# Performance work log

Hardware: AMD Instinct MI355X
Metric: run time of the kernel (lower is better)

## Reference

```python
import jax, jax.numpy as jnp
import numpy as np

N = 40000    # nodes
E = 400000   # edges
H = 128      # hidden_channels
G = 50       # num_gaussians
L = 3        # num_interactions
NG = 256     # number of graphs in the batch
CUTOFF = 6.0


def setup_inputs() -> dict:
    key = jax.random.key(0)
    ks = jax.random.split(key, 16)

    def w(k, shape, fan_in):
        return (jax.random.normal(k, shape, jnp.float32) / np.float32(np.sqrt(fan_in)))

    inp = {}
    inp["atomic_numbers"] = jax.random.randint(ks[0], (N,), 0, 100)
    inp["pos"] = jax.random.normal(ks[1], (N, 3), jnp.float32) * 5.0
    inp["edge_index"] = jax.random.randint(ks[2], (2, E), 0, N)
    inp["batch_ids"] = jnp.sort(jax.random.randint(ks[3], (N,), 0, NG))
    inp["embed"] = w(ks[4], (100, H), 1.0)
    inp["msg_w1"] = w(ks[5], (L, H, H), H)
    inp["msg_b1"] = jnp.zeros((L, H), jnp.float32)
    inp["msg_w2"] = w(ks[6], (L, H, 3 * H), H)
    inp["msg_b2"] = jnp.zeros((L, 3 * H), jnp.float32)
    inp["filt_w"] = w(ks[7], (L, G, 3 * H), G)
    inp["filt_b"] = jnp.zeros((L, 3 * H), jnp.float32)
    inp["vec_w"] = w(ks[8], (L, H, 2 * H), H)
    inp["upd_w1"] = w(ks[9], (L, 2 * H, H), 2 * H)
    inp["upd_b1"] = jnp.zeros((L, H), jnp.float32)
    inp["upd_w2"] = w(ks[10], (L, H, 3 * H), H)
    inp["upd_b2"] = jnp.zeros((L, 3 * H), jnp.float32)
    inp["ro_w1"] = w(ks[11], (H, H // 2), H)
    inp["ro_b1"] = jnp.zeros((H // 2,), jnp.float32)
    inp["ro_w2"] = w(ks[12], (H // 2, 1), H // 2)
    inp["ro_b2"] = jnp.zeros((1,), jnp.float32)
    return inp


def _painn(atomic_numbers, pos, edge_index, batch_ids, embed,
           msg_w1, msg_b1, msg_w2, msg_b2, filt_w, filt_b, vec_w,
           upd_w1, upd_b1, upd_w2, upd_b2, ro_w1, ro_b1, ro_w2, ro_b2):
    src, dst = edge_index[0], edge_index[1]
    n = atomic_numbers.shape[0]

    # geometry
    dvec = pos[src] - pos[dst]                              # [E,3]
    dist = jnp.linalg.norm(dvec, axis=-1)                   # [E]
    dvec_n = dvec / (dist[:, None] + 1e-8)                  # [E,3]

    # Gaussian smearing (RBF expansion of distances)
    offset = jnp.linspace(0.0, CUTOFF, G).astype(jnp.float32)
    coeff = -0.5 / (offset[1] - offset[0]) ** 2
    rbf = jnp.exp(coeff * (dist[:, None] - offset[None, :]) ** 2)  # [E,G]

    s = embed[atomic_numbers]                               # [N,H]
    v = jnp.zeros((n, 3, H), s.dtype)                       # [N,3,H]

    for i in range(L):
        # --- message block ---
        w = rbf @ filt_w[i] + filt_b[i]                     # [E,3H]
        s_all = jax.nn.relu(s @ msg_w1[i] + msg_b1[i]) @ msg_w2[i] + msg_b2[i]  # [N,3H]
        gate = s_all[src] * w                               # [E,3H]
        g0, g1, g2 = jnp.split(gate, 3, axis=-1)            # each [E,H]
        ds_e = g0
        dv_e = v[src] * g1[:, None, :] + dvec_n[:, :, None] * g2[:, None, :]  # [E,3,H]
        ds = jax.ops.segment_sum(ds_e, dst, num_segments=n)
        dv = jax.ops.segment_sum(dv_e, dst, num_segments=n)
        s = s + ds
        v = v + dv

        # --- update block ---
        vt = v @ vec_w[i]                                   # [N,3,2H]
        V1, V2 = jnp.split(vt, 2, axis=-1)                  # [N,3,H] each
        v_norm = jnp.linalg.norm(V1, axis=1)                # [N,H]
        u = (jax.nn.relu(jnp.concatenate([s, v_norm], axis=-1) @ upd_w1[i] + upd_b1[i])
             @ upd_w2[i] + upd_b2[i])                       # [N,3H]
        a, b, c = jnp.split(u, 3, axis=-1)
        s = s + a
        v = v * b[:, None, :] + V2 * c[:, None, :]

    # readout + global mean pool
    y = jax.nn.relu(s @ ro_w1 + ro_b1) @ ro_w2 + ro_b2      # [N,1]
    summed = jax.ops.segment_sum(y, batch_ids, num_segments=NG)
    counts = jax.ops.segment_sum(jnp.ones((n, 1), y.dtype), batch_ids, num_segments=NG)
    return summed / jnp.maximum(counts, 1.0)                # [NG,1]


def reference(atomic_numbers, pos, edge_index, batch_ids, embed,
              msg_w1, msg_b1, msg_w2, msg_b2, filt_w, filt_b, vec_w,
              upd_w1, upd_b1, upd_w2, upd_b2, ro_w1, ro_b1, ro_w2, ro_b2):
    return _painn(atomic_numbers, pos, edge_index, batch_ids, embed,
                  msg_w1, msg_b1, msg_w2, msg_b2, filt_w, filt_b, vec_w,
                  upd_w1, upd_b1, upd_w2, upd_b2, ro_w1, ro_b1, ro_w2, ro_b2)
```

## Files before the change

kernel.cpp:

```cpp
#include <hip/hip_runtime.h>
#include <hip/hip_bf16.h>
#include <math.h>


#define N_NODES 40000
#define N_EDGES 400000
#define NGAUSS  50
#define NLAY    3
#define NGRAPH  256

#define WS_BYTES (448ull * 1024 * 1024)
__device__ __align__(256) unsigned char g_ws[WS_BYTES];

typedef __attribute__((ext_vector_type(8))) short short8;
typedef __attribute__((ext_vector_type(4))) float f32x4;

__device__ __forceinline__ float relu_f(float x) { return fmaxf(x, 0.f); }
__device__ __forceinline__ unsigned short f2b(float x) {
  __hip_bfloat16 h = __float2bfloat16(x);
  return *reinterpret_cast<unsigned short*>(&h);
}
__device__ __forceinline__ float b2f(unsigned short u) {
  return __uint_as_float(((unsigned int)u) << 16);
}
__device__ __forceinline__ float b2f_lo(unsigned int u) {
  return __uint_as_float(u << 16);
}
__device__ __forceinline__ float b2f_hi(unsigned int u) {
  return __uint_as_float(u & 0xffff0000u);
}
__device__ __forceinline__ unsigned int pk(float a, float b) {
  return (unsigned int)f2b(a) | ((unsigned int)f2b(b) << 16);
}
__device__ __forceinline__ int perm384(int c) {
  int j = c >> 7, cc = c & 127;
  return (cc >> 1) * 6 + j * 2 + (cc & 1);
}

#define S0 (NLAY * 128 * 128)
#define S1 (NLAY * 128 * 384)
#define S2 (NLAY * 128 * 256)
#define S3 (NLAY * 256 * 128)
#define S4 (NLAY * 128 * 384)
#define S5 (NLAY * NGAUSS * 384)
#define S6 (128 * 64)
#define S7 (NLAY * 384)
#define S_TOT (S0 + S1 + S2 + S3 + S4 + S5 + S6 + S7)

__global__ __launch_bounds__(256) void cvt_all_kernel(
    const float* __restrict__ m1i, const float* __restrict__ m2i,
    const float* __restrict__ vwi, const float* __restrict__ u1i,
    const float* __restrict__ u2i, const float* __restrict__ fwi,
    const float* __restrict__ roi, const float* __restrict__ mb2i,
    unsigned short* __restrict__ m1o, unsigned short* __restrict__ m2o,
    unsigned short* __restrict__ vwo, unsigned short* __restrict__ u1o,
    unsigned short* __restrict__ u2o, unsigned short* __restrict__ fwo,
    unsigned short* __restrict__ roo, float* __restrict__ mb2o) {
  int i = blockIdx.x * 256 + threadIdx.x;
  if (i >= S_TOT) return;
  if (i < S0) { m1o[i] = f2b(m1i[i]); return; }
  i -= S0;
  if (i < S1) {
    int l = i / (128 * 384), rem = i % (128 * 384);
    int r = rem / 384, c = rem % 384;
    m2o[(size_t)l * 128 * 384 + r * 384 + perm384(c)] = f2b(m2i[i]);
    return;
  }
  i -= S1;
  if (i < S2) { vwo[i] = f2b(vwi[i]); return; }
  i -= S2;
  if (i < S3) { u1o[i] = f2b(u1i[i]); return; }
  i -= S3;
  if (i < S4) { u2o[i] = f2b(u2i[i]); return; }
  i -= S4;
  if (i < S5) {
    int l = i / (NGAUSS * 384), rem = i % (NGAUSS * 384);
    int g = rem / 384, c = rem % 384;
    fwo[(size_t)l * NGAUSS * 384 + g * 384 + perm384(c)] = f2b(fwi[i]);
    return;
  }
  i -= S5;
  if (i < S6) { roo[i] = f2b(roi[i]); return; }
  i -= S6;
  {
    int l = i / 384, c = i % 384;
    mb2o[l * 384 + perm384(c)] = mb2i[i];
  }
}

__global__ __launch_bounds__(256) void geom_kernel(const int* __restrict__ src,
                                                   const int* __restrict__ dst,
                                                   const float* __restrict__ pos,
                                                   float4* __restrict__ geom) {
  int e = blockIdx.x * 256 + threadIdx.x;
  if (e >= N_EDGES) return;
  int s = src[e], d = dst[e];
  float dx = pos[s * 3 + 0] - pos[d * 3 + 0];
  float dy = pos[s * 3 + 1] - pos[d * 3 + 1];
  float dz = pos[s * 3 + 2] - pos[d * 3 + 2];
  float dist = sqrtf(dx * dx + dy * dy + dz * dz);
  float inv = 1.f / (dist + 1e-8f);
  geom[e] = make_float4(dx * inv, dy * inv, dz * inv, dist);
}

__global__ __launch_bounds__(256) void hist_kernel(const int* __restrict__ dst,
                                                   int* __restrict__ deg) {
  int e = blockIdx.x * 256 + threadIdx.x;
  if (e < N_EDGES) atomicAdd(&deg[dst[e]], 1);
}

#define SCAN_NB ((N_NODES + 255) / 256)
__global__ __launch_bounds__(256) void scan_a(const int* __restrict__ deg,
                                              int* __restrict__ bsum) {
  __shared__ int red[4];
  int b = blockIdx.x, t = threadIdx.x;
  int i = b * 256 + t;
  int x = (i < N_NODES) ? deg[i] : 0;
#pragma unroll
  for (int o = 32; o > 0; o >>= 1) x += __shfl_xor(x, o);
  if ((t & 63) == 0) red[t >> 6] = x;
  __syncthreads();
  if (t == 0) bsum[b] = red[0] + red[1] + red[2] + red[3];
}

__global__ __launch_bounds__(64) void scan_b(const int* __restrict__ bsum,
                                             int* __restrict__ boff) {
  int lane = threadIdx.x;
  int carry = 0;
  for (int base = 0; base < SCAN_NB; base += 64) {
    int i = base + lane;
    int v = (i < SCAN_NB) ? bsum[i] : 0;
    int x = v;
#pragma unroll
    for (int d = 1; d < 64; d <<= 1) {
      int y = __shfl_up(x, d);
      if (lane >= d) x += y;
    }
    if (i < SCAN_NB) boff[i] = carry + x - v;
    carry += __shfl(x, 63);
  }
}

__global__ __launch_bounds__(256) void scan_c(const int* __restrict__ deg,
                                              const int* __restrict__ boff,
                                              int* __restrict__ off) {
  __shared__ int woff[4];
  int b = blockIdx.x, t = threadIdx.x, lane = t & 63, w = t >> 6;
  int i = b * 256 + t;
  int v = (i < N_NODES) ? deg[i] : 0;
  int x = v;
#pragma unroll
  for (int d = 1; d < 64; d <<= 1) {
    int y = __shfl_up(x, d);
    if (lane >= d) x += y;
  }
  if (lane == 63) woff[w] = x;
  __syncthreads();
  int add = 0;
  for (int k = 0; k < w; ++k) add += woff[k];
  if (i < N_NODES) off[i] = boff[b] + add + x - v;
  if (b == 0 && t == 0) off[N_NODES] = N_EDGES;
}

__global__ __launch_bounds__(256) void fill_kernel(const int* __restrict__ src,
                                                   const int* __restrict__ dst,
                                                   const int* __restrict__ off,
                                                   int* __restrict__ cursor,
                                                   const float4* __restrict__ geom,
                                                   int* __restrict__ srcs,
                                                   float4* __restrict__ geoms) {
  int e = blockIdx.x * 256 + threadIdx.x;
  if (e >= N_EDGES) return;
  int d = dst[e];
  int p = atomicAdd(&cursor[d], 1);
  int pos = off[d] + p;
  srcs[pos] = src[e];
  geoms[pos] = geom[e];
}

__global__ __launch_bounds__(256) void init_kernel(const int* __restrict__ z,
                                                   const float* __restrict__ embed,
                                                   float* __restrict__ s,
                                                   unsigned short* __restrict__ sb,
                                                   unsigned short* __restrict__ vax) {
  int idx = blockIdx.x * 256 + threadIdx.x;
  if (idx < N_NODES * 384) vax[idx] = 0;
  if (idx < N_NODES * 128) {
    int node = idx >> 7, c = idx & 127;
    float val = embed[z[node] * 128 + c];
    s[idx] = val;
    sb[idx] = f2b(val);
  }
}

template <int BN, int KT>
__global__ __launch_bounds__(256) void gemm_bf16(
    const unsigned short* __restrict__ A1, int lda1,
    const unsigned short* __restrict__ A2, int lda2, int kSplit,
    const unsigned short* __restrict__ B, int ldb,
    const float* __restrict__ bias,
    void* __restrict__ C, int ldc, int M, int K, int doRelu, int outMode) {
  constexpr int NF = BN / 16;
  constexpr int CT = BN / 4;
  __shared__ unsigned int Bt32[BN][KT / 2 + 4];
  int t = threadIdx.x;
  int lane = t & 63, w = t >> 6;
  int n0 = blockIdx.x * BN, m0 = blockIdx.y * 128;
  {
    int c4 = (t & (CT - 1)) * 4;
    int kstep = 2 * (256 / CT);
    for (int k = (t / CT) * 2; k < K; k += kstep) {
      uint2 va = *(const uint2*)&B[(size_t)k * ldb + n0 + c4];
      uint2 vb = *(const uint2*)&B[(size_t)(k + 1) * ldb + n0 + c4];
      Bt32[c4 + 0][k >> 1] = (va.x & 0xffffu) | (vb.x << 16);
      Bt32[c4 + 1][k >> 1] = (va.x >> 16) | (vb.x & 0xffff0000u);
      Bt32[c4 + 2][k >> 1] = (va.y & 0xffffu) | (vb.y << 16);
      Bt32[c4 + 3][k >> 1] = (va.y >> 16) | (vb.y & 0xffff0000u);
    }
  }
  __syncthreads();

  int row = lane & 15;
  int kg = lane >> 4;

  f32x4 acc[2][NF];
#pragma unroll
  for (int rf = 0; rf < 2; ++rf)
#pragma unroll
    for (int nf = 0; nf < NF; ++nf) acc[rf][nf] = (f32x4){0.f, 0.f, 0.f, 0.f};

  for (int ks = 0; ks < K; ks += 32) {
    int kk = ks + kg * 8;
    short8 af[2];
#pragma unroll
    for (int rf = 0; rf < 2; ++rf) {
      int mrow = m0 + w * 32 + rf * 16 + row;
      if (mrow >= M) mrow = M - 1;
      const unsigned short* Ap;
      int kloc;
      if (kk < kSplit) { Ap = A1 + (size_t)mrow * lda1; kloc = kk; }
      else             { Ap = A2 + (size_t)mrow * lda2; kloc = kk - kSplit; }
      af[rf] = *(const short8*)&Ap[kloc];
    }
#pragma unroll
    for (int nf = 0; nf < NF; ++nf) {
      short8 bf = *(const short8*)((const unsigned short*)Bt32[nf * 16 + row] + kk);
#pragma unroll
      for (int rf = 0; rf < 2; ++rf)
        acc[rf][nf] = __builtin_amdgcn_mfma_f32_16x16x32_bf16(af[rf], bf,
                                                              acc[rf][nf], 0, 0, 0);
    }
  }

#pragma unroll
  for (int rf = 0; rf < 2; ++rf)
#pragma unroll
    for (int nf = 0; nf < NF; ++nf)
#pragma unroll
      for (int r = 0; r < 4; ++r) {
        int gr = m0 + w * 32 + rf * 16 + kg * 4 + r;
        int gc = n0 + nf * 16 + row;
        if (gr < M) {
          float val = acc[rf][nf][r] + (bias ? bias[gc] : 0.f);
          if (doRelu) val = relu_f(val);
          if (outMode == 0) ((float*)C)[(size_t)gr * ldc + gc] = val;
          else              ((unsigned short*)C)[(size_t)gr * ldc + gc] = f2b(val);
        }
      }
}

__global__ __launch_bounds__(256) void msg_kernel(const int* __restrict__ off,
                                                  const int* __restrict__ srcs,
                                                  const float4* __restrict__ geoms,
                                                  const unsigned int* __restrict__ s_allX,
                                                  const unsigned int* __restrict__ fwX,
                                                  const float* __restrict__ fb,
                                                  const float* __restrict__ s_in,
                                                  const unsigned int* __restrict__ vAx,
                                                  float* __restrict__ s_out,
                                                  unsigned short* __restrict__ s_out_b,
                                                  unsigned short* __restrict__ v_out_b) {
  int node = blockIdx.x * 4 + (threadIdx.x >> 6);
  if (node >= N_NODES) return;
  int lane = threadIdx.x & 63;
  int c2 = lane * 2;
  const float DELTA = 6.0f / 49.0f;
  const float INVD = 49.0f / 6.0f;
  const float CO = -0.5f * INVD * INVD;
  float fbr[3][2];
#pragma unroll
  for (int jj = 0; jj < 3; ++jj) {
    float2 f = *(const float2*)&fb[jj * 128 + c2];
    fbr[jj][0] = f.x; fbr[jj][1] = f.y;
  }
  float ds[2] = {0.f, 0.f};
  float dv[3][2] = {{0.f}};
  int e0 = off[node], e1 = off[node + 1];

  for (int q = e0; q < e1; ++q) {
    int s = srcs[q];
    float4 gm = geoms[q];
    float d = gm.w;
    float wv[3][2];
#pragma unroll
    for (int jj = 0; jj < 3; ++jj) { wv[jj][0] = fbr[jj][0]; wv[jj][1] = fbr[jj][1]; }
    int glo = max(0, (int)ceilf(d * INVD - 8.f));
    int ghi = min(NGAUSS - 1, (int)floorf(d * INVD + 8.f));
    for (int g = glo; g <= ghi; ++g) {
      float diff = d - g * DELTA;
      float r = __expf(CO * diff * diff);
      const unsigned int* fr = fwX + g * 192 + lane * 3;
      unsigned int f0 = fr[0], f1 = fr[1], f2v = fr[2];
      wv[0][0] = fmaf(r, b2f_lo(f0), wv[0][0]);
      wv[0][1] = fmaf(r, b2f_hi(f0), wv[0][1]);
      wv[1][0] = fmaf(r, b2f_lo(f1), wv[1][0]);
      wv[1][1] = fmaf(r, b2f_hi(f1), wv[1][1]);
      wv[2][0] = fmaf(r, b2f_lo(f2v), wv[2][0]);
      wv[2][1] = fmaf(r, b2f_hi(f2v), wv[2][1]);
    }
    const unsigned int* ps = s_allX + (size_t)s * 192 + lane * 3;
    const unsigned int* pv = vAx + (size_t)s * 192 + lane * 3;
    unsigned int s0 = ps[0], s1 = ps[1], s2 = ps[2];
    unsigned int v0 = pv[0], v1 = pv[1], v2 = pv[2];
    float gt[3][2];
    gt[0][0] = b2f_lo(s0) * wv[0][0];
    gt[0][1] = b2f_hi(s0) * wv[0][1];
    gt[1][0] = b2f_lo(s1) * wv[1][0];
    gt[1][1] = b2f_hi(s1) * wv[1][1];
    gt[2][0] = b2f_lo(s2) * wv[2][0];
    gt[2][1] = b2f_hi(s2) * wv[2][1];
    ds[0] += gt[0][0];
    ds[1] += gt[0][1];
    float dn[3] = {gm.x, gm.y, gm.z};
    unsigned int vvs[3] = {v0, v1, v2};
#pragma unroll
    for (int dd = 0; dd < 3; ++dd) {
      dv[dd][0] = fmaf(b2f_lo(vvs[dd]), gt[1][0], fmaf(dn[dd], gt[2][0], dv[dd][0]));
      dv[dd][1] = fmaf(b2f_hi(vvs[dd]), gt[1][1], fmaf(dn[dd], gt[2][1], dv[dd][1]));
    }
  }

  size_t sb = (size_t)node * 128 + c2;
  float2 si = *(const float2*)&s_in[sb];
  float2 so = make_float2(si.x + ds[0], si.y + ds[1]);
  *(float2*)&s_out[sb] = so;
  *(unsigned int*)&s_out_b[sb] = pk(so.x, so.y);
  const unsigned int* pv0 = vAx + (size_t)node * 192 + lane * 3;
  unsigned int vi0 = pv0[0], vi1 = pv0[1], vi2 = pv0[2];
  unsigned int vis[3] = {vi0, vi1, vi2};
#pragma unroll
  for (int dd = 0; dd < 3; ++dd) {
    size_t vb = (size_t)node * 384 + dd * 128 + c2;
    float vo0 = b2f_lo(vis[dd]) + dv[dd][0];
    float vo1 = b2f_hi(vis[dd]) + dv[dd][1];
    *(unsigned int*)&v_out_b[vb] = pk(vo0, vo1);
  }
}

__global__ __launch_bounds__(256) void vnorm_kernel(const unsigned short* __restrict__ V12b,
                                                    unsigned short* __restrict__ vnb) {
  int idx = blockIdx.x * 256 + threadIdx.x;
  if (idx >= N_NODES * 32) return;
  int node = idx >> 5, c4 = (idx & 31) * 4;
  size_t b = (size_t)node * 768 + c4;
  ushort4 x = *(const ushort4*)&V12b[b];
  ushort4 y = *(const ushort4*)&V12b[b + 256];
  ushort4 zz = *(const ushort4*)&V12b[b + 512];
  ushort4 o;
  o.x = f2b(sqrtf(b2f(x.x) * b2f(x.x) + b2f(y.x) * b2f(y.x) + b2f(zz.x) * b2f(zz.x)));
  o.y = f2b(sqrtf(b2f(x.y) * b2f(x.y) + b2f(y.y) * b2f(y.y) + b2f(zz.y) * b2f(zz.y)));
  o.z = f2b(sqrtf(b2f(x.z) * b2f(x.z) + b2f(y.z) * b2f(y.z) + b2f(zz.z) * b2f(zz.z)));
  o.w = f2b(sqrtf(b2f(x.w) * b2f(x.w) + b2f(y.w) * b2f(y.w) + b2f(zz.w) * b2f(zz.w)));
  *(ushort4*)&vnb[(size_t)node * 128 + c4] = o;
}

__global__ __launch_bounds__(256) void update_kernel(const float* __restrict__ s_msg,
                                                     const unsigned short* __restrict__ v_msg_b,
                                                     const unsigned short* __restrict__ u_b,
                                                     const unsigned short* __restrict__ V12b,
                                                     float* __restrict__ s_out,
                                                     unsigned short* __restrict__ s_out_b,
                                                     unsigned int* __restrict__ vAx) {
  int idx = blockIdx.x * 256 + threadIdx.x;
  if (idx >= N_NODES * 32) return;
  int node = idx >> 5, c4 = (idx & 31) * 4;
  size_t ub = (size_t)node * 384 + c4;
  ushort4 a4 = *(const ushort4*)&u_b[ub];
  ushort4 b4 = *(const ushort4*)&u_b[ub + 128];
  ushort4 c4v = *(const ushort4*)&u_b[ub + 256];
  size_t sb = (size_t)node * 128 + c4;
  float4 sm = *(const float4*)&s_msg[sb];
  float4 so = make_float4(sm.x + b2f(a4.x), sm.y + b2f(a4.y),
                          sm.z + b2f(a4.z), sm.w + b2f(a4.w));
  *(float4*)&s_out[sb] = so;
  ushort4 sob = {f2b(so.x), f2b(so.y), f2b(so.z), f2b(so.w)};
  *(ushort4*)&s_out_b[sb] = sob;
  float bb[4] = {b2f(b4.x), b2f(b4.y), b2f(b4.z), b2f(b4.w)};
  float cc[4] = {b2f(c4v.x), b2f(c4v.y), b2f(c4v.z), b2f(c4v.w)};
  int l0 = c4 >> 1;
#pragma unroll
  for (int dd = 0; dd < 3; ++dd) {
    size_t vb = (size_t)node * 384 + dd * 128 + c4;
    size_t vbv = (size_t)node * 768 + dd * 256 + 128 + c4;
    ushort4 vm = *(const ushort4*)&v_msg_b[vb];
    ushort4 v2 = *(const ushort4*)&V12b[vbv];
    float o0 = b2f(vm.x) * bb[0] + b2f(v2.x) * cc[0];
    float o1 = b2f(vm.y) * bb[1] + b2f(v2.y) * cc[1];
    float o2 = b2f(vm.z) * bb[2] + b2f(v2.z) * cc[2];
    float o3 = b2f(vm.w) * bb[3] + b2f(v2.w) * cc[3];
    vAx[(size_t)node * 192 + l0 * 3 + dd] = pk(o0, o1);
    vAx[(size_t)node * 192 + (l0 + 1) * 3 + dd] = pk(o2, o3);
  }
}

__global__ __launch_bounds__(256) void readout2_kernel(const float* __restrict__ ro_h,
                                                       const float* __restrict__ w2,
                                                       float* __restrict__ y) {
  int node = blockIdx.x * 4 + (threadIdx.x >> 6);
  if (node >= N_NODES) return;
  int lane = threadIdx.x & 63;
  float v = ro_h[(size_t)node * 64 + lane] * w2[lane];
#pragma unroll
  for (int o = 32; o > 0; o >>= 1) v += __shfl_xor(v, o);
  if (lane == 0) y[node] = v;
}

__global__ __launch_bounds__(64) void pool_kernel(const float* __restrict__ y,
                                                  const int* __restrict__ batch,
                                                  const float* __restrict__ b2,
                                                  float* __restrict__ out) {
  int g = blockIdx.x;
  int lane = threadIdx.x;
  int s, e;
  {
    int lo = 0, hi = N_NODES;
    while (lo < hi) { int mid = (lo + hi) >> 1; if (batch[mid] < g) lo = mid + 1; else hi = mid; }
    s = lo;
    lo = s; hi = N_NODES;
    while (lo < hi) { int mid = (lo + hi) >> 1; if (batch[mid] < g + 1) lo = mid + 1; else hi = mid; }
    e = lo;
  }
  float acc = 0.f;
  for (int i = s + lane; i < e; i += 64) acc += y[i];
#pragma unroll
  for (int o = 32; o > 0; o >>= 1) acc += __shfl_xor(acc, o);
  if (lane == 0) {
    float c = (float)(e - s);
    out[g] = (acc + c * b2[0]) / fmaxf(c, 1.f);
  }
}

extern "C" void kernel_launch(void* const* d_in, const int* in_sizes, int n_in,
                              void* d_out, int out_size, void* d_ws, size_t ws_size,
                              hipStream_t stream) {
  const int*   z      = (const int*)d_in[0];
  const float* pos    = (const float*)d_in[1];
  const int*   esrc   = (const int*)d_in[2];
  const int*   edst   = esrc + N_EDGES;
  const int*   batch  = (const int*)d_in[3];
  const float* embed  = (const float*)d_in[4];
  const float* msg_w1 = (const float*)d_in[5];
  const float* msg_b1 = (const float*)d_in[6];
  const float* msg_w2 = (const float*)d_in[7];
  const float* msg_b2 = (const float*)d_in[8];
  const float* filt_w = (const float*)d_in[9];
  const float* filt_b = (const float*)d_in[10];
  const float* vec_w  = (const float*)d_in[11];
  const float* upd_w1 = (const float*)d_in[12];
  const float* upd_b1 = (const float*)d_in[13];
  const float* upd_w2 = (const float*)d_in[14];
  const float* upd_b2 = (const float*)d_in[15];
  const float* ro_w1  = (const float*)d_in[16];
  const float* ro_b1  = (const float*)d_in[17];
  const float* ro_w2  = (const float*)d_in[18];
  const float* ro_b2  = (const float*)d_in[19];
  (void)in_sizes; (void)n_in; (void)out_size;

  void* wsp = nullptr;
  if (hipGetSymbolAddress(&wsp, HIP_SYMBOL(g_ws)) != hipSuccess || wsp == nullptr) {
    wsp = d_ws;
  }
  char* wsb = (char*)wsp;
  size_t o = 0;
  auto alloc = [&](size_t bytes) -> void* {
    void* p = wsb + o;
    o += (bytes + 255) & ~(size_t)255;
    return p;
  };
  float4* geom   = (float4*)alloc(sizeof(float4) * N_EDGES);
  float4* geoms  = (float4*)alloc(sizeof(float4) * N_EDGES);
  int* srcs      = (int*)alloc(4ull * N_EDGES);
  int* csr_off   = (int*)alloc(4ull * (N_NODES + 1));
  int* deg       = (int*)alloc(4ull * N_NODES);
  int* cursor    = (int*)alloc(4ull * N_NODES);
  int* bsum      = (int*)alloc(4ull * SCAN_NB);
  int* boff      = (int*)alloc(4ull * SCAN_NB);
  float* sA      = (float*)alloc(4ull * N_NODES * 128);
  float* sB      = (float*)alloc(4ull * N_NODES * 128);
  float* ro_h    = (float*)alloc(4ull * N_NODES * 64);
  float* ybuf    = (float*)alloc(4ull * N_NODES);
  float* mb2p    = (float*)alloc(4ull * NLAY * 384);
  unsigned short* s_allX = (unsigned short*)alloc(2ull * N_NODES * 384);
  unsigned short* sAb    = (unsigned short*)alloc(2ull * N_NODES * 128);
  unsigned short* sBb    = (unsigned short*)alloc(2ull * N_NODES * 128);
  unsigned short* vAx    = (unsigned short*)alloc(2ull * N_NODES * 384);
  unsigned short* vBb    = (unsigned short*)alloc(2ull * N_NODES * 384);
  unsigned short* vnb    = (unsigned short*)alloc(2ull * N_NODES * 128);
  unsigned short* hidden = (unsigned short*)alloc(2ull * N_NODES * 128);
  unsigned short* Vbuf_b = (unsigned short*)alloc(2ull * N_NODES * 768);
  unsigned short* ubuf_b = (unsigned short*)alloc(2ull * N_NODES * 384);
  unsigned short* wb_m1  = (unsigned short*)alloc(2ull * S0);
  unsigned short* wb_m2  = (unsigned short*)alloc(2ull * S1);
  unsigned short* wb_vw  = (unsigned short*)alloc(2ull * S2);
  unsigned short* wb_u1  = (unsigned short*)alloc(2ull * S3);
  unsigned short* wb_u2  = (unsigned short*)alloc(2ull * S4);
  unsigned short* wb_fwX = (unsigned short*)alloc(2ull * S5);
  unsigned short* wb_ro  = (unsigned short*)alloc(2ull * S6);

  if (wsb == (char*)d_ws && o > ws_size) return;

  hipMemsetAsync(deg, 0, 4ull * N_NODES, stream);
  hipMemsetAsync(cursor, 0, 4ull * N_NODES, stream);

  cvt_all_kernel<<<(S_TOT + 255) / 256, 256, 0, stream>>>(
      msg_w1, msg_w2, vec_w, upd_w1, upd_w2, filt_w, ro_w1, msg_b2,
      wb_m1, wb_m2, wb_vw, wb_u1, wb_u2, wb_fwX, wb_ro, mb2p);

  geom_kernel<<<(N_EDGES + 255) / 256, 256, 0, stream>>>(esrc, edst, pos, geom);
  hist_kernel<<<(N_EDGES + 255) / 256, 256, 0, stream>>>(edst, deg);
  scan_a<<<SCAN_NB, 256, 0, stream>>>(deg, bsum);
  scan_b<<<1, 64, 0, stream>>>(bsum, boff);
  scan_c<<<SCAN_NB, 256, 0, stream>>>(deg, boff, csr_off);
  fill_kernel<<<(N_EDGES + 255) / 256, 256, 0, stream>>>(esrc, edst, csr_off, cursor,
                                                         geom, srcs, geoms);
  init_kernel<<<(N_NODES * 384 + 255) / 256, 256, 0, stream>>>(z, embed, sA, sAb, vAx);

  const int BIG = 1 << 30;
  const int GY40 = (N_NODES + 127) / 128;
  const int GY120 = (N_NODES * 3 + 127) / 128;
  for (int i = 0; i < NLAY; ++i) {
    const float* mb1 = msg_b1 + (size_t)i * 128;
    const float* mb2i = mb2p + (size_t)i * 384;
    const float* fbv = filt_b + (size_t)i * 384;
    const float* ub1 = upd_b1 + (size_t)i * 128;
    const float* ub2 = upd_b2 + (size_t)i * 384;
    const unsigned short* m1 = wb_m1 + (size_t)i * 128 * 128;
    const unsigned short* m2 = wb_m2 + (size_t)i * 128 * 384;
    const unsigned short* vw = wb_vw + (size_t)i * 128 * 256;
    const unsigned short* u1 = wb_u1 + (size_t)i * 256 * 128;
    const unsigned short* u2 = wb_u2 + (size_t)i * 128 * 384;
    const unsigned int* fwX = (const unsigned int*)(wb_fwX + (size_t)i * 50 * 384);

    gemm_bf16<64, 128><<<dim3(2, GY40), 256, 0, stream>>>(sAb, 128, sAb, 128, BIG, m1,
                                                          128, mb1, hidden, 128,
                                                          N_NODES, 128, 1, 1);
    gemm_bf16<128, 128><<<dim3(3, GY40), 256, 0, stream>>>(hidden, 128, hidden, 128,
                                                           BIG, m2, 384, mb2i, s_allX,
                                                           384, N_NODES, 128, 0, 1);
    msg_kernel<<<N_NODES / 4, 256, 0, stream>>>(csr_off, srcs, geoms,
                                                (const unsigned int*)s_allX, fwX, fbv,
                                                sA, (const unsigned int*)vAx,
                                                sB, sBb, vBb);
    gemm_bf16<128, 128><<<dim3(2, GY120), 256, 0, stream>>>(vBb, 128, vBb, 128, BIG,
                                                            vw, 256, nullptr, Vbuf_b,
                                                            256, N_NODES * 3, 128,
                                                            0, 1);
    vnorm_kernel<<<(N_NODES * 32 + 255) / 256, 256, 0, stream>>>(Vbuf_b, vnb);
    gemm_bf16<64, 256><<<dim3(2, GY40), 256, 0, stream>>>(sBb, 128, vnb, 128, 128, u1,
                                                          128, ub1, hidden, 128,
                                                          N_NODES, 256, 1, 1);
    gemm_bf16<128, 128><<<dim3(3, GY40), 256, 0, stream>>>(hidden, 128, hidden, 128,
                                                           BIG, u2, 384, ub2, ubuf_b,
                                                           384, N_NODES, 128, 0, 1);
    update_kernel<<<(N_NODES * 32 + 255) / 256, 256, 0, stream>>>(sB, vBb, ubuf_b,
                                                                  Vbuf_b, sA, sAb,
                                                                  (unsigned int*)vAx);
  }

  gemm_bf16<64, 128><<<dim3(1, GY40), 256, 0, stream>>>(sAb, 128, sAb, 128, BIG, wb_ro,
                                                        64, ro_b1, ro_h, 64, N_NODES,
                                                        128, 1, 0);
  readout2_kernel<<<N_NODES / 4, 256, 0, stream>>>(ro_h, wb_ro ? ro_w2 : ro_w2, ybuf);
  pool_kernel<<<NGRAPH, 64, 0, stream>>>(ybuf, batch, ro_b2, (float*)d_out);
}
```

Before: 1.103 ms.

## Interleave scalar filter and vector features per node; fuse geometry into CSR fill

The per-node scalar message features and vector state now share one interleaved buffer (768 bf16 per node), so each gathered neighbour in the message kernel reads one contiguous 1.5KB region instead of two separate rows. The geometry kernel is folded into the CSR fill kernel, which removes one launch and an intermediate float4 edge array. The trade-off is a wider row stride for the GEMM output and for vector writes in the update kernel, and an unused parameter left in the message kernel.

Result: no change. 1.089 ms (-1.2%).

```diff
diff --git a/kernel.cpp b/kernel.cpp
--- a/kernel.cpp
+++ b/kernel.cpp
@@ -88,10 +88,72 @@
   }
 }
 
-__global__ __launch_bounds__(256) void geom_kernel(const int* __restrict__ src,
+__global__ __launch_bounds__(256) void hist_kernel(const int* __restrict__ dst,
+                                                   int* __restrict__ deg) {
+  int e = blockIdx.x * 256 + threadIdx.x;
+  if (e < N_EDGES) atomicAdd(&deg[dst[e]], 1);
+}
+
+#define SCAN_NB ((N_NODES + 255) / 256)
+__global__ __launch_bounds__(256) void scan_a(const int* __restrict__ deg,
+                                              int* __restrict__ bsum) {
+  __shared__ int red[4];
+  int b = blockIdx.x, t = threadIdx.x;
+  int i = b * 256 + t;
+  int x = (i < N_NODES) ? deg[i] : 0;
+#pragma unroll
+  for (int o = 32; o > 0; o >>= 1) x += __shfl_xor(x, o);
+  if ((t & 63) == 0) red[t >> 6] = x;
+  __syncthreads();
+  if (t == 0) bsum[b] = red[0] + red[1] + red[2] + red[3];
+}
+
+__global__ __launch_bounds__(64) void scan_b(const int* __restrict__ bsum,
+                                             int* __restrict__ boff) {
+  int lane = threadIdx.x;
+  int carry = 0;
+  for (int base = 0; base < SCAN_NB; base += 64) {
+    int i = base + lane;
+    int v = (i < SCAN_NB) ? bsum[i] : 0;
+    int x = v;
+#pragma unroll
+    for (int d = 1; d < 64; d <<= 1) {
+      int y = __shfl_up(x, d);
+      if (lane >= d) x += y;
+    }
+    if (i < SCAN_NB) boff[i] = carry + x - v;
+    carry += __shfl(x, 63);
+  }
+}
+
+__global__ __launch_bounds__(256) void scan_c(const int* __restrict__ deg,
+                                              const int* __restrict__ boff,
+                                              int* __restrict__ off) {
+  __shared__ int woff[4];
+  int b = blockIdx.x, t = threadIdx.x, lane = t & 63, w = t >> 6;
+  int i = b * 256 + t;
+  int v = (i < N_NODES) ? deg[i] : 0;
+  int x = v;
+#pragma unroll
+  for (int d = 1; d < 64; d <<= 1) {
+    int y = __shfl_up(x, d);
+    if (lane >= d) x += y;
+  }
+  if (lane == 63) woff[w] = x;
+  __syncthreads();
+  int add = 0;
+  for (int k = 0; k < w; ++k) add += woff[k];
+  if (i < N_NODES) off[i] = boff[b] + add + x - v;
+  if (b == 0 && t == 0) off[N_NODES] = N_EDGES;
+}
+
+__global__ __launch_bounds__(256) void fill_kernel(const int* __restrict__ src,
                                                    const int* __restrict__ dst,
+                                                   const int* __restrict__ off,
+                                                   int* __restrict__ cursor,
                                                    const float* __restrict__ pos,
-                                                   float4* __restrict__ geom) {
+                                                   int* __restrict__ srcs,
+                                                   float4* __restrict__ geoms) {
   int e = blockIdx.x * 256 + threadIdx.x;
   if (e >= N_EDGES) return;
   int s = src[e], d = dst[e];
@@ -100,91 +162,22 @@
   float dz = pos[s * 3 + 2] - pos[d * 3 + 2];
   float dist = sqrtf(dx * dx + dy * dy + dz * dz);
   float inv = 1.f / (dist + 1e-8f);
-  geom[e] = make_float4(dx * inv, dy * inv, dz * inv, dist);
-}
-
-__global__ __launch_bounds__(256) void hist_kernel(const int* __restrict__ dst,
-                                                   int* __restrict__ deg) {
-  int e = blockIdx.x * 256 + threadIdx.x;
-  if (e < N_EDGES) atomicAdd(&deg[dst[e]], 1);
-}
-
-#define SCAN_NB ((N_NODES + 255) / 256)
-__global__ __launch_bounds__(256) void scan_a(const int* __restrict__ deg,
-                                              int* __restrict__ bsum) {
-  __shared__ int red[4];
-  int b = blockIdx.x, t = threadIdx.x;
-  int i = b * 256 + t;
-  int x = (i < N_NODES) ? deg[i] : 0;
-#pragma unroll
-  for (int o = 32; o > 0; o >>= 1) x += __shfl_xor(x, o);
-  if ((t & 63) == 0) red[t >> 6] = x;
-  __syncthreads();
-  if (t == 0) bsum[b] = red[0] + red[1] + red[2] + red[3];
-}
-
-__global__ __launch_bounds__(64) void scan_b(const int* __restrict__ bsum,
-                                             int* __restrict__ boff) {
-  int lane = threadIdx.x;
-  int carry = 0;
-  for (int base = 0; base < SCAN_NB; base += 64) {
-    int i = base + lane;
-    int v = (i < SCAN_NB) ? bsum[i] : 0;
-    int x = v;
-#pragma unroll
-    for (int d = 1; d < 64; d <<= 1) {
-      int y = __shfl_up(x, d);
-      if (lane >= d) x += y;
-    }
-    if (i < SCAN_NB) boff[i] = carry + x - v;
-    carry += __shfl(x, 63);
-  }
-}
-
-__global__ __launch_bounds__(256) void scan_c(const int* __restrict__ deg,
-                                              const int* __restrict__ boff,
-                                              int* __restrict__ off) {
-  __shared__ int woff[4];
-  int b = blockIdx.x, t = threadIdx.x, lane = t & 63, w = t >> 6;
-  int i = b * 256 + t;
-  int v = (i < N_NODES) ? deg[i] : 0;
-  int x = v;
-#pragma unroll
-  for (int d = 1; d < 64; d <<= 1) {
-    int y = __shfl_up(x, d);
-    if (lane >= d) x += y;
-  }
-  if (lane == 63) woff[w] = x;
-  __syncthreads();
-  int add = 0;
-  for (int k = 0; k < w; ++k) add += woff[k];
-  if (i < N_NODES) off[i] = boff[b] + add + x - v;
-  if (b == 0 && t == 0) off[N_NODES] = N_EDGES;
-}
-
-__global__ __launch_bounds__(256) void fill_kernel(const int* __restrict__ src,
-                                                   const int* __restrict__ dst,
-                                                   const int* __restrict__ off,
-                                                   int* __restrict__ cursor,
-                                                   const float4* __restrict__ geom,
-                                                   int* __restrict__ srcs,
-                                                   float4* __restrict__ geoms) {
-  int e = blockIdx.x * 256 + threadIdx.x;
-  if (e >= N_EDGES) return;
-  int d = dst[e];
   int p = atomicAdd(&cursor[d], 1);
-  int pos = off[d] + p;
-  srcs[pos] = src[e];
-  geoms[pos] = geom[e];
+  int q = off[d] + p;
+  srcs[q] = s;
+  geoms[q] = make_float4(dx * inv, dy * inv, dz * inv, dist);
 }
 
 __global__ __launch_bounds__(256) void init_kernel(const int* __restrict__ z,
                                                    const float* __restrict__ embed,
                                                    float* __restrict__ s,
                                                    unsigned short* __restrict__ sb,
-                                                   unsigned short* __restrict__ vax) {
+                                                   unsigned short* __restrict__ sv) {
   int idx = blockIdx.x * 256 + threadIdx.x;
-  if (idx < N_NODES * 384) vax[idx] = 0;
+  if (idx < N_NODES * 384) {
+    int node = idx / 384, c = idx % 384;
+    sv[(size_t)node * 768 + 384 + c] = 0;
+  }
   if (idx < N_NODES * 128) {
     int node = idx >> 7, c = idx & 127;
     float val = embed[z[node] * 128 + c];
@@ -272,14 +265,14 @@
 __global__ __launch_bounds__(256) void msg_kernel(const int* __restrict__ off,
                                                   const int* __restrict__ srcs,
                                                   const float4* __restrict__ geoms,
-                                                  const unsigned int* __restrict__ s_allX,
+                                                  const unsigned int* __restrict__ sv,
                                                   const unsigned int* __restrict__ fwX,
                                                   const float* __restrict__ fb,
                                                   const float* __restrict__ s_in,
-                                                  const unsigned int* __restrict__ vAx,
                                                   float* __restrict__ s_out,
                                                   unsigned short* __restrict__ s_out_b,
-                                                  unsigned short* __restrict__ v_out_b) {
+                                                  unsigned short* __restrict__ v_out_b,
+                                                  unsigned int* __restrict__ sv_v_out) {
   int node = blockIdx.x * 4 + (threadIdx.x >> 6);
   if (node >= N_NODES) return;
   int lane = threadIdx.x & 63;
@@ -318,10 +311,9 @@
       wv[2][0] = fmaf(r, b2f_lo(f2v), wv[2][0]);
       wv[2][1] = fmaf(r, b2f_hi(f2v), wv[2][1]);
     }
-    const unsigned int* ps = s_allX + (size_t)s * 192 + lane * 3;
-    const unsigned int* pv = vAx + (size_t)s * 192 + lane * 3;
-    unsigned int s0 = ps[0], s1 = ps[1], s2 = ps[2];
-    unsigned int v0 = pv[0], v1 = pv[1], v2 = pv[2];
+    const unsigned int* base = sv + (size_t)s * 384 + lane * 3;
+    unsigned int s0 = base[0], s1 = base[1], s2 = base[2];
+    unsigned int v0 = base[192], v1 = base[193], v2 = base[194];
     float gt[3][2];
     gt[0][0] = b2f_lo(s0) * wv[0][0];
     gt[0][1] = b2f_hi(s0) * wv[0][1];
@@ -345,7 +337,7 @@
   float2 so = make_float2(si.x + ds[0], si.y + ds[1]);
   *(float2*)&s_out[sb] = so;
   *(unsigned int*)&s_out_b[sb] = pk(so.x, so.y);
-  const unsigned int* pv0 = vAx + (size_t)node * 192 + lane * 3;
+  const unsigned int* pv0 = sv + (size_t)node * 384 + 192 + lane * 3;
   unsigned int vi0 = pv0[0], vi1 = pv0[1], vi2 = pv0[2];
   unsigned int vis[3] = {vi0, vi1, vi2};
 #pragma unroll
@@ -355,6 +347,7 @@
     float vo1 = b2f_hi(vis[dd]) + dv[dd][1];
     *(unsigned int*)&v_out_b[vb] = pk(vo0, vo1);
   }
+  (void)sv_v_out;
 }
 
 __global__ __launch_bounds__(256) void vnorm_kernel(const unsigned short* __restrict__ V12b,
@@ -380,7 +373,7 @@
                                                      const unsigned short* __restrict__ V12b,
                                                      float* __restrict__ s_out,
                                                      unsigned short* __restrict__ s_out_b,
-                                                     unsigned int* __restrict__ vAx) {
+                                                     unsigned int* __restrict__ sv) {
   int idx = blockIdx.x * 256 + threadIdx.x;
   if (idx >= N_NODES * 32) return;
   int node = idx >> 5, c4 = (idx & 31) * 4;
@@ -408,8 +401,8 @@
     float o1 = b2f(vm.y) * bb[1] + b2f(v2.y) * cc[1];
     float o2 = b2f(vm.z) * bb[2] + b2f(v2.z) * cc[2];
     float o3 = b2f(vm.w) * bb[3] + b2f(v2.w) * cc[3];
-    vAx[(size_t)node * 192 + l0 * 3 + dd] = pk(o0, o1);
-    vAx[(size_t)node * 192 + (l0 + 1) * 3 + dd] = pk(o2, o3);
+    sv[(size_t)node * 384 + 192 + l0 * 3 + dd] = pk(o0, o1);
+    sv[(size_t)node * 384 + 192 + (l0 + 1) * 3 + dd] = pk(o2, o3);
   }
 }
 
@@ -487,7 +480,6 @@
     o += (bytes + 255) & ~(size_t)255;
     return p;
   };
-  float4* geom   = (float4*)alloc(sizeof(float4) * N_EDGES);
   float4* geoms  = (float4*)alloc(sizeof(float4) * N_EDGES);
   int* srcs      = (int*)alloc(4ull * N_EDGES);
   int* csr_off   = (int*)alloc(4ull * (N_NODES + 1));
@@ -500,10 +492,9 @@
   float* ro_h    = (float*)alloc(4ull * N_NODES * 64);
   float* ybuf    = (float*)alloc(4ull * N_NODES);
   float* mb2p    = (float*)alloc(4ull * NLAY * 384);
-  unsigned short* s_allX = (unsigned short*)alloc(2ull * N_NODES * 384);
+  unsigned short* svX    = (unsigned short*)alloc(2ull * N_NODES * 768);
   unsigned short* sAb    = (unsigned short*)alloc(2ull * N_NODES * 128);
   unsigned short* sBb    = (unsigned short*)alloc(2ull * N_NODES * 128);
-  unsigned short* vAx    = (unsigned short*)alloc(2ull * N_NODES * 384);
   unsigned short* vBb    = (unsigned short*)alloc(2ull * N_NODES * 384);
   unsigned short* vnb    = (unsigned short*)alloc(2ull * N_NODES * 128);
   unsigned short* hidden = (unsigned short*)alloc(2ull * N_NODES * 128);
@@ -526,14 +517,13 @@
       msg_w1, msg_w2, vec_w, upd_w1, upd_w2, filt_w, ro_w1, msg_b2,
       wb_m1, wb_m2, wb_vw, wb_u1, wb_u2, wb_fwX, wb_ro, mb2p);
 
-  geom_kernel<<<(N_EDGES + 255) / 256, 256, 0, stream>>>(esrc, edst, pos, geom);
   hist_kernel<<<(N_EDGES + 255) / 256, 256, 0, stream>>>(edst, deg);
   scan_a<<<SCAN_NB, 256, 0, stream>>>(deg, bsum);
   scan_b<<<1, 64, 0, stream>>>(bsum, boff);
   scan_c<<<SCAN_NB, 256, 0, stream>>>(deg, boff, csr_off);
   fill_kernel<<<(N_EDGES + 255) / 256, 256, 0, stream>>>(esrc, edst, csr_off, cursor,
-                                                         geom, srcs, geoms);
-  init_kernel<<<(N_NODES * 384 + 255) / 256, 256, 0, stream>>>(z, embed, sA, sAb, vAx);
+                                                         pos, srcs, geoms);
+  init_kernel<<<(N_NODES * 384 + 255) / 256, 256, 0, stream>>>(z, embed, sA, sAb, svX);
 
   const int BIG = 1 << 30;
   const int GY40 = (N_NODES + 127) / 128;
@@ -555,12 +545,11 @@
                                                           128, mb1, hidden, 128,
                                                           N_NODES, 128, 1, 1);
     gemm_bf16<128, 128><<<dim3(3, GY40), 256, 0, stream>>>(hidden, 128, hidden, 128,
-                                                           BIG, m2, 384, mb2i, s_allX,
-                                                           384, N_NODES, 128, 0, 1);
+                                                           BIG, m2, 384, mb2i, svX,
+                                                           768, N_NODES, 128, 0, 1);
     msg_kernel<<<N_NODES / 4, 256, 0, stream>>>(csr_off, srcs, geoms,
-                                                (const unsigned int*)s_allX, fwX, fbv,
-                                                sA, (const unsigned int*)vAx,
-                                                sB, sBb, vBb);
+                                                (const unsigned int*)svX, fwX, fbv,
+                                                sA, sB, sBb, vBb, (unsigned int*)svX);
     gemm_bf16<128, 128><<<dim3(2, GY120), 256, 0, stream>>>(vBb, 128, vBb, 128, BIG,
                                                             vw, 256, nullptr, Vbuf_b,
                                                             256, N_NODES * 3, 128,
@@ -574,12 +563,12 @@
                                                            384, N_NODES, 128, 0, 1);
     update_kernel<<<(N_NODES * 32 + 255) / 256, 256, 0, stream>>>(sB, vBb, ubuf_b,
                                                                   Vbuf_b, sA, sAb,
-                                                                  (unsigned int*)vAx);
+                                                                  (unsigned int*)svX);
   }
 
   gemm_bf16<64, 128><<<dim3(1, GY40), 256, 0, stream>>>(sAb, 128, sAb, 128, BIG, wb_ro,
                                                         64, ro_b1, ro_h, 64, N_NODES,
                                                         128, 1, 0);
-  readout2_kernel<<<N_NODES / 4, 256, 0, stream>>>(ro_h, wb_ro ? ro_w2 : ro_w2, ybuf);
+  readout2_kernel<<<N_NODES / 4, 256, 0, stream>>>(ro_h, ro_w2, ybuf);
   pool_kernel<<<NGRAPH, 64, 0, stream>>>(ybuf, batch, ro_b2, (float*)d_out);
 }
```
